# Kernel optimization log

Hardware: AMD Instinct MI355X
Metric: run time of the kernel (lower is better)

The kernel has to match this reference:

```python
import jax, jax.numpy as jnp
import numpy as np

N_NODES = 50000
N_EDGES = 800000
ATOM_F = 64
NBR_F = 64
EPS = 1e-5


def batch_norm(x, gamma, beta):
    # BatchNorm1d in training mode: batch stats, biased variance
    mu = x.mean(axis=0)
    var = x.var(axis=0)
    return gamma * (x - mu) * jax.lax.rsqrt(var + EPS) + beta


def setup_inputs() -> dict:
    key = jax.random.key(0)
    ks = jax.random.split(key, 8)
    d_in = 2 * ATOM_F + NBR_F  # 192
    d_out = 2 * ATOM_F         # 128
    return {
        "atom_in_fea": jax.random.normal(ks[0], (N_NODES, ATOM_F), dtype=jnp.float32),
        "nbr_fea": jax.random.normal(ks[1], (N_EDGES, NBR_F), dtype=jnp.float32),
        "edge_src": jax.random.randint(ks[2], (N_EDGES,), 0, N_NODES),
        "edge_dst": jax.random.randint(ks[3], (N_EDGES,), 0, N_NODES),
        "W_full": jax.random.normal(ks[4], (d_in, d_out), dtype=jnp.float32) / np.sqrt(d_in),
        "b_full": jnp.zeros((d_out,), dtype=jnp.float32),
        "bn1_g": jnp.ones((d_out,), dtype=jnp.float32),
        "bn1_b": jnp.zeros((d_out,), dtype=jnp.float32),
        "bn2_g": jnp.ones((ATOM_F,), dtype=jnp.float32),
        "bn2_b": jnp.zeros((ATOM_F,), dtype=jnp.float32),
    }


def reference(atom_in_fea, nbr_fea, edge_src, edge_dst,
              W_full, b_full, bn1_g, bn1_b, bn2_g, bn2_b):
    # gather endpoint features per edge: [E, 2*A + Nf]
    atom_src = atom_in_fea[edge_src]
    atom_dst = atom_in_fea[edge_dst]
    total = jnp.concatenate([atom_src, atom_dst, nbr_fea], axis=1)
    total = batch_norm(total @ W_full + b_full, bn1_g, bn1_b)  # [E, 2*A]
    filter_fea, core_fea = jnp.split(total, 2, axis=1)
    nbr_msg = jax.nn.sigmoid(filter_fea) * jax.nn.softplus(core_fea)  # [E, A]
    # scatter-add messages back to destination nodes
    atom_update = jax.ops.segment_sum(nbr_msg, edge_dst, num_segments=atom_in_fea.shape[0])
    return jax.nn.softplus(atom_in_fea + batch_norm(atom_update, bn2_g, bn2_b))
```

## Files before the change

### kernel.cpp

```cpp
#include <hip/hip_runtime.h>
#include <hip/hip_fp16.h>
#include <math.h>

#define N_NODES 50000
#define N_EDGES 800000
#define ATOMF 64
#define DIN 192
#define DOUT 128
#define EPB 64
#define NTILES (N_EDGES / EPB)
#define LDW 200
#define NSLOT (EPB * 25)

typedef __attribute__((ext_vector_type(8))) short bf16x8;
typedef __attribute__((ext_vector_type(8))) short s16x8;
typedef __attribute__((ext_vector_type(4))) float f32x4;

__device__ __forceinline__ short f2bf(float f) {
  unsigned u = __float_as_uint(f);
  u += 0x7fffu + ((u >> 16) & 1u);
  return (short)(u >> 16);
}
__device__ __forceinline__ float bf2f(unsigned short u) {
  return __uint_as_float(((unsigned)u) << 16);
}
__device__ __forceinline__ unsigned short f2h(float f) {
  __half h = __float2half_rn(f);
  return *(unsigned short*)&h;
}
__device__ __forceinline__ float h2f(unsigned short u) {
  __half h = *(__half*)&u;
  return __half2float(h);
}
__device__ __forceinline__ float softplus_f(float x) {
  return fmaxf(x, 0.f) + log1pf(__expf(-fabsf(x)));
}
__device__ __forceinline__ float sigmoid_f(float x) {
  return 1.f / (1.f + __expf(-x));
}
__device__ __forceinline__ float fast_sigmoid(float x) {
  return __builtin_amdgcn_rcpf(1.f + __expf(-x));
}
__device__ __forceinline__ float fast_softplus(float x) {
  return fmaxf(x, 0.f) + __logf(1.f + __expf(-fabsf(x)));
}

#define GLOAD16(g, l)                                                          \
  __builtin_amdgcn_global_load_lds(                                            \
      (const __attribute__((address_space(1))) void*)(g),                      \
      (__attribute__((address_space(3))) void*)(l), 16, 0, 0)

__launch_bounds__(256)
__global__ void precvt_k(const float* __restrict__ atom,
                         const float* __restrict__ nbr,
                         unsigned short* __restrict__ atom_bf,
                         unsigned short* __restrict__ nbr_bf) {
  const int NA = N_NODES * ATOMF / 8;
  const int NB = N_EDGES * ATOMF / 8;
  int stride = gridDim.x * blockDim.x;
  for (int i = blockIdx.x * blockDim.x + threadIdx.x; i < NA + NB; i += stride) {
    const float* s;
    unsigned short* d;
    if (i < NA) { s = atom + (size_t)i * 8; d = atom_bf + (size_t)i * 8; }
    else        { s = nbr + (size_t)(i - NA) * 8; d = nbr_bf + (size_t)(i - NA) * 8; }
    float4 a = ((const float4*)s)[0];
    float4 b = ((const float4*)s)[1];
    s16x8 t;
    t[0] = f2bf(a.x); t[1] = f2bf(a.y); t[2] = f2bf(a.z); t[3] = f2bf(a.w);
    t[4] = f2bf(b.x); t[5] = f2bf(b.y); t[6] = f2bf(b.z); t[7] = f2bf(b.w);
    *(s16x8*)d = t;
  }
}

__launch_bounds__(256)
__global__ void hist_k(const int* __restrict__ edst, int* __restrict__ deg) {
  int gid = blockIdx.x * 256 + threadIdx.x;
  if (gid < N_EDGES) atomicAdd(&deg[edst[gid]], 1);
}

__launch_bounds__(1024)
__global__ void scan_k(const int* __restrict__ deg,
                       int* __restrict__ rowptr,
                       int* __restrict__ cursor) {
  __shared__ int wsum[16];
  const int tid = threadIdx.x;
  const int lane = tid & 63, wv = tid >> 6;
  int base = 0;
  for (int c0 = 0; c0 < N_NODES; c0 += 1024) {
    int i = c0 + tid;
    int v = (i < N_NODES) ? deg[i] : 0;
    int s = v;
    #pragma unroll
    for (int d = 1; d < 64; d <<= 1) {
      int t = __shfl_up(s, d, 64);
      if (lane >= d) s += t;
    }
    if (lane == 63) wsum[wv] = s;
    __syncthreads();
    if (wv == 0 && lane < 16) {
      int ws = wsum[lane];
      #pragma unroll
      for (int d = 1; d < 16; d <<= 1) {
        int t = __shfl_up(ws, d, 64);
        if (lane >= d) ws += t;
      }
      wsum[lane] = ws;
    }
    __syncthreads();
    int wbase = wv ? wsum[wv - 1] : 0;
    int excl = base + wbase + s - v;
    if (i < N_NODES) { rowptr[i] = excl; cursor[i] = excl; }
    int tot = wsum[15];
    __syncthreads();
    base += tot;
  }
  if (tid == 0) rowptr[N_NODES] = base;
}

__launch_bounds__(256)
__global__ void fill_k(const int* __restrict__ edst,
                       int* __restrict__ cursor,
                       int* __restrict__ perm) {
  int gid = blockIdx.x * 256 + threadIdx.x;
  if (gid < N_EDGES) {
    int pos = atomicAdd(&cursor[edst[gid]], 1);
    perm[pos] = gid;
  }
}

__device__ __forceinline__ void stage_tile(const unsigned short* __restrict__ atom_bf,
                                           const unsigned short* __restrict__ nbr_bf,
                                           const int* __restrict__ esrc,
                                           const int* __restrict__ edst,
                                           int e0, unsigned short* lbase,
                                           const int* g_enc, int wv) {
  #pragma unroll
  for (int it = 0; it < 7; ++it) {
    if (it * 256 + wv * 64 < NSLOT) {
      int e = g_enc[it];
      int row = e & 255;
      int coff = (e >> 8) & 255;
      int sel = e >> 16;
      const unsigned short* src;
      if (sel < 2) {
        const int* ip = sel ? edst : esrc;
        int idx = ip[e0 + row];
        src = atom_bf + (size_t)idx * ATOMF + coff;
      } else {
        src = nbr_bf + (size_t)(e0 + row) * ATOMF + coff;
      }
      GLOAD16(src, lbase + (size_t)(it * 256 + wv * 64) * 8);
    }
  }
}

__launch_bounds__(256, 4)
__global__ void edge_gemm(const unsigned short* __restrict__ atom_bf,
                          const unsigned short* __restrict__ nbr_bf,
                          const int* __restrict__ esrc,
                          const int* __restrict__ edst,
                          const float* __restrict__ W,
                          float* __restrict__ stats,
                          unsigned short* __restrict__ zt) {
  __shared__ unsigned short Tl[EPB * LDW];

  const int tid = threadIdx.x;
  const int lane = tid & 63;
  const int wv = tid >> 6;
  const int l15 = lane & 15;
  const int lg = lane >> 4;
  const int colF = wv * 16 + l15;
  const int colC = colF + 64;

  bf16x8 wf[2][6];
  #pragma unroll
  for (int cg = 0; cg < 2; ++cg) {
    #pragma unroll
    for (int kk = 0; kk < 6; ++kk) {
      bf16x8 t;
      #pragma unroll
      for (int jj = 0; jj < 8; ++jj)
        t[jj] = f2bf(W[(size_t)(kk * 32 + lg * 8 + jj) * 128 + cg * 64 + colF]);
      wf[cg][kk] = t;
    }
  }

  int g_enc[7];
  #pragma unroll
  for (int it = 0; it < 7; ++it) {
    int s = it * 256 + tid;
    if (s >= NSLOT) s = 0;
    int row = s / 25;
    int w = s - row * 25;
    int sel, coff;
    if (w < 8)       { sel = 0; coff = w * 8; }
    else if (w < 16) { sel = 1; coff = (w - 8) * 8; }
    else             { sel = 2; coff = (w < 24 ? (w - 16) * 8 : 0); }
    g_enc[it] = row | (coff << 8) | (sel << 16);
  }

  float fs[2] = {0.f, 0.f}, fq[2] = {0.f, 0.f};

  for (int tile = blockIdx.x; tile < NTILES; tile += gridDim.x) {
    stage_tile(atom_bf, nbr_bf, esrc, edst, tile * EPB, Tl, g_enc, wv);
    __syncthreads();

    f32x4 acc[2][4] = {};
    #pragma unroll
    for (int rg = 0; rg < 4; ++rg) {
      #pragma unroll
      for (int kk = 0; kk < 6; ++kk) {
        bf16x8 a = *(const bf16x8*)&Tl[(rg * 16 + l15) * LDW + kk * 32 + lg * 8];
        acc[0][rg] = __builtin_amdgcn_mfma_f32_16x16x32_bf16(a, wf[0][kk], acc[0][rg], 0, 0, 0);
        acc[1][rg] = __builtin_amdgcn_mfma_f32_16x16x32_bf16(a, wf[1][kk], acc[1][rg], 0, 0, 0);
      }
    }

    #pragma unroll
    for (int cg = 0; cg < 2; ++cg) {
      unsigned short* zb = zt + ((size_t)tile * 128 + cg * 64 + colF) * 64 + lg * 4;
      #pragma unroll
      for (int rg = 0; rg < 4; ++rg) {
        float z0 = acc[cg][rg][0], z1 = acc[cg][rg][1];
        float z2 = acc[cg][rg][2], z3 = acc[cg][rg][3];
        fs[cg] += (z0 + z1) + (z2 + z3);
        fq[cg] += z0 * z0 + z1 * z1 + z2 * z2 + z3 * z3;
        uint2 p;
        p.x = (unsigned)f2h(z0) | ((unsigned)f2h(z1) << 16);
        p.y = (unsigned)f2h(z2) | ((unsigned)f2h(z3) << 16);
        *(uint2*)(zb + rg * 16) = p;
      }
    }
    __syncthreads();
  }

  #pragma unroll
  for (int cg = 0; cg < 2; ++cg) {
    fs[cg] += __shfl_xor(fs[cg], 16, 64); fs[cg] += __shfl_xor(fs[cg], 32, 64);
    fq[cg] += __shfl_xor(fq[cg], 16, 64); fq[cg] += __shfl_xor(fq[cg], 32, 64);
  }
  if (lane < 16) {
    atomicAdd(&stats[colF], fs[0]);
    atomicAdd(&stats[colC], fs[1]);
    atomicAdd(&stats[128 + colF], fq[0]);
    atomicAdd(&stats[128 + colC], fq[1]);
  }
}

__global__ void finalize1_k(const float* __restrict__ stats,
                            const float* __restrict__ g,
                            const float* __restrict__ be,
                            float* __restrict__ ab) {
  int n = threadIdx.x;
  float mu = stats[n] * (1.f / N_EDGES);
  float var = stats[128 + n] * (1.f / N_EDGES) - mu * mu;
  float a = g[n] * rsqrtf(var + 1e-5f);
  ab[n] = a;
  ab[128 + n] = be[n] - mu * a;
}

__launch_bounds__(256)
__global__ void msg_k(const unsigned short* __restrict__ zt,
                      const float* __restrict__ ab,
                      unsigned short* __restrict__ msg) {
  __shared__ unsigned short ml[64][72];
  const int tile = blockIdx.x;
  const int tid = threadIdx.x;
  const int c = tid & 63;
  const int rg = tid >> 6;
  const unsigned short* fb = zt + ((size_t)tile * 128 + c) * 64 + rg * 16;
  const unsigned short* gb = fb + (size_t)64 * 64;
  s16x8 f0 = *(const s16x8*)fb;
  s16x8 f1 = *(const s16x8*)(fb + 8);
  s16x8 g0 = *(const s16x8*)gb;
  s16x8 g1 = *(const s16x8*)(gb + 8);
  float af = ab[c], cf = ab[128 + c];
  float ag = ab[64 + c], cg = ab[192 + c];
  #pragma unroll
  for (int k = 0; k < 16; ++k) {
    unsigned short fu = (unsigned short)(k < 8 ? f0[k] : f1[k - 8]);
    unsigned short gu = (unsigned short)(k < 8 ? g0[k] : g1[k - 8]);
    float f = af * h2f(fu) + cf;
    float g = ag * h2f(gu) + cg;
    ml[rg * 16 + k][c] = f2h(fast_sigmoid(f) * fast_softplus(g));
  }
  __syncthreads();
  const int r = tid >> 2;
  const int cq = (tid & 3) * 16;
  s16x8 o0, o1;
  #pragma unroll
  for (int k = 0; k < 8; ++k) { o0[k] = ml[r][cq + k]; o1[k] = ml[r][cq + 8 + k]; }
  unsigned short* ob = msg + ((size_t)tile * 64 + r) * 64 + cq;
  *(s16x8*)ob = o0;
  *(s16x8*)(ob + 8) = o1;
}

__launch_bounds__(256)
__global__ void gather_k(const unsigned short* __restrict__ msg,
                         const int* __restrict__ rowptr,
                         const int* __restrict__ perm,
                         float* __restrict__ out) {
  int n = blockIdx.x * 4 + (threadIdx.x >> 6);
  if (n >= N_NODES) return;
  int lane = threadIdx.x & 63;
  int s = rowptr[n], e = rowptr[n + 1];
  float acc = 0.f;
  for (int i = s; i < e; ++i) {
    int ed = perm[i];
    acc += h2f(msg[(size_t)ed * 64 + lane]);
  }
  out[(size_t)n * 64 + lane] = acc;
}

__launch_bounds__(256)
__global__ void stats2_k(const float* __restrict__ upd, float* __restrict__ stats2) {
  int tid = threadIdx.x;
  int gid = blockIdx.x * 256 + tid;
  int stride = gridDim.x * 256;
  float4 s = make_float4(0.f, 0.f, 0.f, 0.f);
  float4 q = make_float4(0.f, 0.f, 0.f, 0.f);
  for (int i = gid; i < N_NODES * 16; i += stride) {
    float4 v = ((const float4*)upd)[i];
    s.x += v.x; s.y += v.y; s.z += v.z; s.w += v.w;
    q.x += v.x * v.x; q.y += v.y * v.y; q.z += v.z * v.z; q.w += v.w * v.w;
  }
  int lane = tid & 63;
  int wv = tid >> 6;
  s.x += __shfl_xor(s.x, 16, 64); s.x += __shfl_xor(s.x, 32, 64);
  s.y += __shfl_xor(s.y, 16, 64); s.y += __shfl_xor(s.y, 32, 64);
  s.z += __shfl_xor(s.z, 16, 64); s.z += __shfl_xor(s.z, 32, 64);
  s.w += __shfl_xor(s.w, 16, 64); s.w += __shfl_xor(s.w, 32, 64);
  q.x += __shfl_xor(q.x, 16, 64); q.x += __shfl_xor(q.x, 32, 64);
  q.y += __shfl_xor(q.y, 16, 64); q.y += __shfl_xor(q.y, 32, 64);
  q.z += __shfl_xor(q.z, 16, 64); q.z += __shfl_xor(q.z, 32, 64);
  q.w += __shfl_xor(q.w, 16, 64); q.w += __shfl_xor(q.w, 32, 64);
  __shared__ float red[4 * 128];
  if (lane < 16) {
    int f = lane * 4;
    red[wv * 128 + f + 0] = s.x; red[wv * 128 + f + 1] = s.y;
    red[wv * 128 + f + 2] = s.z; red[wv * 128 + f + 3] = s.w;
    red[wv * 128 + 64 + f + 0] = q.x; red[wv * 128 + 64 + f + 1] = q.y;
    red[wv * 128 + 64 + f + 2] = q.z; red[wv * 128 + 64 + f + 3] = q.w;
  }
  __syncthreads();
  if (tid < 128) {
    float v = red[tid] + red[128 + tid] + red[256 + tid] + red[384 + tid];
    atomicAdd(&stats2[tid], v);
  }
}

__global__ void finalize2_k(const float* __restrict__ stats2,
                            const float* __restrict__ g,
                            const float* __restrict__ be,
                            float* __restrict__ ab2) {
  int f = threadIdx.x;
  float mu = stats2[f] * (1.f / N_NODES);
  float var = stats2[64 + f] * (1.f / N_NODES) - mu * mu;
  float a = g[f] * rsqrtf(var + 1e-5f);
  ab2[f] = a;
  ab2[64 + f] = be[f] - mu * a;
}

__launch_bounds__(256)
__global__ void out_k(const float* __restrict__ atom,
                      const float* __restrict__ ab2,
                      float* __restrict__ out) {
  int gid = blockIdx.x * 256 + threadIdx.x;
  int stride = gridDim.x * 256;
  for (int i = gid; i < N_NODES * 16; i += stride) {
    float4 u = ((const float4*)out)[i];
    float4 x = ((const float4*)atom)[i];
    int f = (i & 15) * 4;
    float4 r;
    r.x = softplus_f(x.x + u.x * ab2[f + 0] + ab2[64 + f + 0]);
    r.y = softplus_f(x.y + u.y * ab2[f + 1] + ab2[64 + f + 1]);
    r.z = softplus_f(x.z + u.z * ab2[f + 2] + ab2[64 + f + 2]);
    r.w = softplus_f(x.w + u.w * ab2[f + 3] + ab2[64 + f + 3]);
    ((float4*)out)[i] = r;
  }
}

__launch_bounds__(256)
__global__ void scatter_k(const unsigned short* __restrict__ zt,
                          const int* __restrict__ edst,
                          const float* __restrict__ ab,
                          float* __restrict__ out) {
  int gid = blockIdx.x * 256 + threadIdx.x;
  int r8 = gid & 7;
  int c = (gid >> 3) & 63;
  int tile = gid >> 9;
  const unsigned short* fb = zt + ((size_t)tile * 128 + c) * 64 + r8 * 8;
  const unsigned short* gb = fb + 64 * 64;
  s16x8 f8 = *(const s16x8*)fb;
  s16x8 g8 = *(const s16x8*)gb;
  float af = ab[c], cf = ab[128 + c];
  float ag = ab[64 + c], cg = ab[192 + c];
  int4 d0 = *(const int4*)(edst + tile * 64 + r8 * 8);
  int4 d1 = *(const int4*)(edst + tile * 64 + r8 * 8 + 4);
  int dsts[8] = {d0.x, d0.y, d0.z, d0.w, d1.x, d1.y, d1.z, d1.w};
  #pragma unroll
  for (int i = 0; i < 8; ++i) {
    float f = af * h2f((unsigned short)f8[i]) + cf;
    float g = ag * h2f((unsigned short)g8[i]) + cg;
    float m = sigmoid_f(f) * softplus_f(g);
    atomicAdd(out + (size_t)dsts[i] * ATOMF + c, m);
  }
}

template<int PASS>
__launch_bounds__(256, 2)
__global__ void edge_pass(const float* __restrict__ atom,
                          const float* __restrict__ nbr,
                          const int* __restrict__ esrc,
                          const int* __restrict__ edst,
                          const float* __restrict__ W,
                          const float* __restrict__ bvec,
                          float* __restrict__ stats,
                          const float* __restrict__ ab,
                          float* __restrict__ upd) {
  __shared__ short Wl[DOUT * LDW];
  __shared__ short Tl[EPB * LDW];
  __shared__ int eix[2 * EPB];

  const int tid = threadIdx.x;
  const int lane = tid & 63;
  const int wv = tid >> 6;
  const int l15 = lane & 15;
  const int lg = lane >> 4;

  for (int i = tid; i < DIN * DOUT; i += 256) {
    int k = i >> 7, n = i & 127;
    Wl[n * LDW + k] = f2bf(W[i]);
  }
  float bcol[8], acol[8], ccol[8];
  #pragma unroll
  for (int j = 0; j < 8; ++j) {
    int n = j * 16 + l15;
    bcol[j] = bvec[n];
    if constexpr (PASS == 1) { acol[j] = ab[n]; ccol[j] = ab[DOUT + n]; }
    else { acol[j] = 0.f; ccol[j] = 0.f; }
  }
  float fsum[8], fsq[8];
  #pragma unroll
  for (int j = 0; j < 8; ++j) { fsum[j] = 0.f; fsq[j] = 0.f; }

  for (int tile = blockIdx.x; tile < NTILES; tile += gridDim.x) {
    const int e0 = tile * EPB;
    __syncthreads();
    if (tid < EPB) eix[tid] = esrc[e0 + tid];
    else if (tid < 2 * EPB) eix[tid] = edst[e0 + tid - EPB];
    __syncthreads();
    for (int i = tid; i < EPB * 96; i += 256) {
      int row = i / 96;
      int cl = (i - row * 96) * 2;
      const float* p;
      if (cl < 64)       p = atom + (size_t)eix[row] * 64 + cl;
      else if (cl < 128) p = atom + (size_t)eix[EPB + row] * 64 + (cl - 64);
      else               p = nbr + (size_t)(e0 + row) * 64 + (cl - 128);
      float2 v = *(const float2*)p;
      unsigned pk = (unsigned)(unsigned short)f2bf(v.x)
                  | ((unsigned)(unsigned short)f2bf(v.y) << 16);
      *(unsigned*)&Tl[row * LDW + cl] = pk;
    }
    __syncthreads();
    f32x4 acc[8] = {};
    const int abase = (wv * 16 + l15) * LDW + lg * 8;
    #pragma unroll
    for (int kk = 0; kk < 6; ++kk) {
      bf16x8 afr = *(const bf16x8*)&Tl[abase + kk * 32];
      #pragma unroll
      for (int j = 0; j < 8; ++j) {
        bf16x8 bfr = *(const bf16x8*)&Wl[(j * 16 + l15) * LDW + lg * 8 + kk * 32];
        acc[j] = __builtin_amdgcn_mfma_f32_16x16x32_bf16(afr, bfr, acc[j], 0, 0, 0);
      }
    }
    if constexpr (PASS == 0) {
      #pragma unroll
      for (int j = 0; j < 8; ++j)
        #pragma unroll
        for (int r = 0; r < 4; ++r) {
          float z = acc[j][r] + bcol[j];
          fsum[j] += z; fsq[j] += z * z;
        }
    } else {
      #pragma unroll
      for (int r = 0; r < 4; ++r) {
        int row = wv * 16 + lg * 4 + r;
        int d = eix[EPB + row];
        float* urow = upd + (size_t)d * 64;
        #pragma unroll
        for (int j = 0; j < 4; ++j) {
          float f = (acc[j][r] + bcol[j]) * acol[j] + ccol[j];
          float g = (acc[j + 4][r] + bcol[j + 4]) * acol[j + 4] + ccol[j + 4];
          atomicAdd(&urow[j * 16 + l15], sigmoid_f(f) * softplus_f(g));
        }
      }
    }
  }
  if constexpr (PASS == 0) {
    #pragma unroll
    for (int j = 0; j < 8; ++j) {
      fsum[j] += __shfl_xor(fsum[j], 16, 64);
      fsum[j] += __shfl_xor(fsum[j], 32, 64);
      fsq[j]  += __shfl_xor(fsq[j], 16, 64);
      fsq[j]  += __shfl_xor(fsq[j], 32, 64);
    }
    __syncthreads();
    float* redf = (float*)Tl;
    if (lane < 16) {
      #pragma unroll
      for (int j = 0; j < 8; ++j) {
        redf[wv * 256 + j * 16 + lane] = fsum[j];
        redf[wv * 256 + 128 + j * 16 + lane] = fsq[j];
      }
    }
    __syncthreads();
    float s = redf[tid] + redf[256 + tid] + redf[512 + tid] + redf[768 + tid];
    atomicAdd(&stats[tid], s);
  }
}

extern "C" void kernel_launch(void* const* d_in, const int* in_sizes, int n_in,
                              void* d_out, int out_size, void* d_ws, size_t ws_size,
                              hipStream_t stream) {
  const float* atom = (const float*)d_in[0];
  const float* nbr  = (const float*)d_in[1];
  const int*   esrc = (const int*)d_in[2];
  const int*   edst = (const int*)d_in[3];
  const float* W    = (const float*)d_in[4];
  const float* bvec = (const float*)d_in[5];
  const float* g1   = (const float*)d_in[6];
  const float* b1   = (const float*)d_in[7];
  const float* g2   = (const float*)d_in[8];
  const float* b2   = (const float*)d_in[9];
  float* out = (float*)d_out;
  char* ws = (char*)d_ws;

  float* stats1 = (float*)ws;
  float* ab1    = stats1 + 256;
  float* stats2 = stats1 + 512;
  float* ab2    = stats1 + 640;

  const size_t OFF_ATOM = 4096;
  const size_t SZ_ATOM  = (size_t)N_NODES * ATOMF * 2;
  const size_t OFF_NBR  = OFF_ATOM + SZ_ATOM;
  const size_t SZ_NBR   = (size_t)N_EDGES * ATOMF * 2;
  const size_t OFF_ZT   = OFF_NBR + SZ_NBR;
  const size_t SZ_ZT    = (size_t)N_EDGES * DOUT * 2;
  const size_t NEED_OLD = OFF_ZT + SZ_ZT;
  const size_t OFF_PERM = NEED_OLD;
  const size_t SZ_PERM  = (size_t)N_EDGES * 4;
  const size_t OFF_DEG  = OFF_PERM + SZ_PERM;
  const size_t OFF_RP   = OFF_DEG + N_NODES * 4;
  const size_t OFF_CUR  = OFF_RP + (N_NODES + 1) * 4 + 12;
  const size_t NEED_NEW = OFF_CUR + N_NODES * 4;

  hipMemsetAsync(stats1, 0, 768 * sizeof(float), stream);

  if (ws_size >= NEED_NEW) {
    unsigned short* atom_bf = (unsigned short*)(ws + OFF_ATOM);
    unsigned short* nbr_bf  = (unsigned short*)(ws + OFF_NBR);
    unsigned short* zt      = (unsigned short*)(ws + OFF_ZT);
    unsigned short* msg     = nbr_bf;
    int* perm   = (int*)(ws + OFF_PERM);
    int* deg    = (int*)(ws + OFF_DEG);
    int* rowptr = (int*)(ws + OFF_RP);
    int* cursor = (int*)(ws + OFF_CUR);

    hipMemsetAsync(deg, 0, N_NODES * sizeof(int), stream);
    hist_k<<<(N_EDGES + 255) / 256, 256, 0, stream>>>(edst, deg);
    scan_k<<<1, 1024, 0, stream>>>(deg, rowptr, cursor);
    fill_k<<<(N_EDGES + 255) / 256, 256, 0, stream>>>(edst, cursor, perm);

    precvt_k<<<2048, 256, 0, stream>>>(atom, nbr, atom_bf, nbr_bf);
    edge_gemm<<<1024, 256, 0, stream>>>(atom_bf, nbr_bf, esrc, edst, W, stats1, zt);
    finalize1_k<<<1, 128, 0, stream>>>(stats1, g1, b1, ab1);

    msg_k<<<NTILES, 256, 0, stream>>>(zt, ab1, msg);
    gather_k<<<(N_NODES + 3) / 4, 256, 0, stream>>>(msg, rowptr, perm, out);
  } else if (ws_size >= NEED_OLD) {
    unsigned short* atom_bf = (unsigned short*)(ws + OFF_ATOM);
    unsigned short* nbr_bf  = (unsigned short*)(ws + OFF_NBR);
    unsigned short* zt      = (unsigned short*)(ws + OFF_ZT);
    hipMemsetAsync(out, 0, (size_t)N_NODES * 64 * sizeof(float), stream);
    precvt_k<<<2048, 256, 0, stream>>>(atom, nbr, atom_bf, nbr_bf);
    edge_gemm<<<1024, 256, 0, stream>>>(atom_bf, nbr_bf, esrc, edst, W, stats1, zt);
    finalize1_k<<<1, 128, 0, stream>>>(stats1, g1, b1, ab1);
    scatter_k<<<25000, 256, 0, stream>>>(zt, edst, ab1, out);
  } else {
    hipMemsetAsync(out, 0, (size_t)N_NODES * 64 * sizeof(float), stream);
    edge_pass<0><<<512, 256, 0, stream>>>(atom, nbr, esrc, edst, W, bvec,
                                          stats1, nullptr, nullptr);
    finalize1_k<<<1, 128, 0, stream>>>(stats1, g1, b1, ab1);
    edge_pass<1><<<512, 256, 0, stream>>>(atom, nbr, esrc, edst, W, bvec,
                                          nullptr, ab1, out);
  }

  stats2_k<<<512, 256, 0, stream>>>(out, stats2);
  finalize2_k<<<1, 64, 0, stream>>>(stats2, g2, b2, ab2);
  out_k<<<512, 256, 0, stream>>>(atom, ab2, out);
}
```

Baseline: 552.7 us.

## Scatter messages into CSR order and prefetch next edge tile in GEMM

fill_k now records each edge's destination-sorted position (inverse permutation) instead of the permutation. msg_k writes each message row directly into its sorted slot, so gather_k reads contiguous rows without the perm indirection. edge_gemm stages the next tile into shared memory right after the MFMA loop, so those loads overlap the output stores, and it raises occupancy to 6 blocks per SM with a 1536-block grid. In exchange msg_k's writes become scattered rows, and the tighter launch bound may cause register spills.

Result: slower. 751.6 us (+36.0%).

```diff
diff --git a/kernel.cpp b/kernel.cpp
--- a/kernel.cpp
+++ b/kernel.cpp
@@ -120,11 +120,11 @@
 __launch_bounds__(256)
 __global__ void fill_k(const int* __restrict__ edst,
                        int* __restrict__ cursor,
-                       int* __restrict__ perm) {
+                       int* __restrict__ iperm) {
   int gid = blockIdx.x * 256 + threadIdx.x;
   if (gid < N_EDGES) {
     int pos = atomicAdd(&cursor[edst[gid]], 1);
-    perm[pos] = gid;
+    iperm[gid] = pos;
   }
 }
 
@@ -154,7 +154,7 @@
   }
 }
 
-__launch_bounds__(256, 4)
+__launch_bounds__(256, 6)
 __global__ void edge_gemm(const unsigned short* __restrict__ atom_bf,
                           const unsigned short* __restrict__ nbr_bf,
                           const int* __restrict__ esrc,
@@ -201,8 +201,11 @@
 
   float fs[2] = {0.f, 0.f}, fq[2] = {0.f, 0.f};
 
-  for (int tile = blockIdx.x; tile < NTILES; tile += gridDim.x) {
-    stage_tile(atom_bf, nbr_bf, esrc, edst, tile * EPB, Tl, g_enc, wv);
+  int t0 = blockIdx.x;
+  if (t0 < NTILES)
+    stage_tile(atom_bf, nbr_bf, esrc, edst, t0 * EPB, Tl, g_enc, wv);
+
+  for (int tile = t0; tile < NTILES; tile += gridDim.x) {
     __syncthreads();
 
     f32x4 acc[2][4] = {};
@@ -215,6 +218,11 @@
         acc[1][rg] = __builtin_amdgcn_mfma_f32_16x16x32_bf16(a, wf[1][kk], acc[1][rg], 0, 0, 0);
       }
     }
+    __syncthreads();
+
+    int nxt = tile + gridDim.x;
+    if (nxt < NTILES)
+      stage_tile(atom_bf, nbr_bf, esrc, edst, nxt * EPB, Tl, g_enc, wv);
 
     #pragma unroll
     for (int cg = 0; cg < 2; ++cg) {
@@ -231,7 +239,6 @@
         *(uint2*)(zb + rg * 16) = p;
       }
     }
-    __syncthreads();
   }
 
   #pragma unroll
@@ -262,6 +269,7 @@
 __launch_bounds__(256)
 __global__ void msg_k(const unsigned short* __restrict__ zt,
                       const float* __restrict__ ab,
+                      const int* __restrict__ iperm,
                       unsigned short* __restrict__ msg) {
   __shared__ unsigned short ml[64][72];
   const int tile = blockIdx.x;
@@ -284,13 +292,14 @@
     float g = ag * h2f(gu) + cg;
     ml[rg * 16 + k][c] = f2h(fast_sigmoid(f) * fast_softplus(g));
   }
+  const int r = tid >> 2;
+  const int pos = iperm[tile * 64 + r];
   __syncthreads();
-  const int r = tid >> 2;
   const int cq = (tid & 3) * 16;
   s16x8 o0, o1;
   #pragma unroll
   for (int k = 0; k < 8; ++k) { o0[k] = ml[r][cq + k]; o1[k] = ml[r][cq + 8 + k]; }
-  unsigned short* ob = msg + ((size_t)tile * 64 + r) * 64 + cq;
+  unsigned short* ob = msg + (size_t)pos * 64 + cq;
   *(s16x8*)ob = o0;
   *(s16x8*)(ob + 8) = o1;
 }
@@ -298,17 +307,14 @@
 __launch_bounds__(256)
 __global__ void gather_k(const unsigned short* __restrict__ msg,
                          const int* __restrict__ rowptr,
-                         const int* __restrict__ perm,
                          float* __restrict__ out) {
   int n = blockIdx.x * 4 + (threadIdx.x >> 6);
   if (n >= N_NODES) return;
   int lane = threadIdx.x & 63;
   int s = rowptr[n], e = rowptr[n + 1];
   float acc = 0.f;
-  for (int i = s; i < e; ++i) {
-    int ed = perm[i];
-    acc += h2f(msg[(size_t)ed * 64 + lane]);
-  }
+  for (int i = s; i < e; ++i)
+    acc += h2f(msg[(size_t)i * 64 + lane]);
   out[(size_t)n * 64 + lane] = acc;
 }
 
@@ -562,7 +568,7 @@
     unsigned short* nbr_bf  = (unsigned short*)(ws + OFF_NBR);
     unsigned short* zt      = (unsigned short*)(ws + OFF_ZT);
     unsigned short* msg     = nbr_bf;
-    int* perm   = (int*)(ws + OFF_PERM);
+    int* iperm  = (int*)(ws + OFF_PERM);
     int* deg    = (int*)(ws + OFF_DEG);
     int* rowptr = (int*)(ws + OFF_RP);
     int* cursor = (int*)(ws + OFF_CUR);
@@ -570,21 +576,21 @@
     hipMemsetAsync(deg, 0, N_NODES * sizeof(int), stream);
     hist_k<<<(N_EDGES + 255) / 256, 256, 0, stream>>>(edst, deg);
     scan_k<<<1, 1024, 0, stream>>>(deg, rowptr, cursor);
-    fill_k<<<(N_EDGES + 255) / 256, 256, 0, stream>>>(edst, cursor, perm);
+    fill_k<<<(N_EDGES + 255) / 256, 256, 0, stream>>>(edst, cursor, iperm);
 
     precvt_k<<<2048, 256, 0, stream>>>(atom, nbr, atom_bf, nbr_bf);
-    edge_gemm<<<1024, 256, 0, stream>>>(atom_bf, nbr_bf, esrc, edst, W, stats1, zt);
+    edge_gemm<<<1536, 256, 0, stream>>>(atom_bf, nbr_bf, esrc, edst, W, stats1, zt);
     finalize1_k<<<1, 128, 0, stream>>>(stats1, g1, b1, ab1);
 
-    msg_k<<<NTILES, 256, 0, stream>>>(zt, ab1, msg);
-    gather_k<<<(N_NODES + 3) / 4, 256, 0, stream>>>(msg, rowptr, perm, out);
+    msg_k<<<NTILES, 256, 0, stream>>>(zt, ab1, iperm, msg);
+    gather_k<<<(N_NODES + 3) / 4, 256, 0, stream>>>(msg, rowptr, out);
   } else if (ws_size >= NEED_OLD) {
     unsigned short* atom_bf = (unsigned short*)(ws + OFF_ATOM);
     unsigned short* nbr_bf  = (unsigned short*)(ws + OFF_NBR);
     unsigned short* zt      = (unsigned short*)(ws + OFF_ZT);
     hipMemsetAsync(out, 0, (size_t)N_NODES * 64 * sizeof(float), stream);
     precvt_k<<<2048, 256, 0, stream>>>(atom, nbr, atom_bf, nbr_bf);
-    edge_gemm<<<1024, 256, 0, stream>>>(atom_bf, nbr_bf, esrc, edst, W, stats1, zt);
+    edge_gemm<<<1536, 256, 0, stream>>>(atom_bf, nbr_bf, esrc, edst, W, stats1, zt);
     finalize1_k<<<1, 128, 0, stream>>>(stats1, g1, b1, ab1);
     scatter_k<<<25000, 256, 0, stream>>>(zt, edst, ab1, out);
   } else {
```
